# Kernel tuning notes

Measured on AMD Instinct MI355X. Metric: run time of the kernel, lower is better.

Reference implementation:

```python
import jax, jax.numpy as jnp
import numpy as np
from jax.scipy.special import ndtr, logsumexp

K = 2  # top-k experts (init kwarg k=2)


def setup_inputs() -> dict:
    key = jax.random.key(0)
    k1, k2, k3, k4 = jax.random.split(key, 4)
    B, D, E = 131072, 1024, 64
    x_flat = jax.random.normal(k1, (B, D), jnp.float32)
    # Original inits w_gate/w_noise to zeros; use small random weights so
    # top-k routing is non-degenerate for correctness testing.
    w_gate = jax.random.normal(k2, (D, E), jnp.float32) * 0.02
    w_noise = jax.random.normal(k3, (D, E), jnp.float32) * 0.02
    eps = jax.random.normal(k4, (B, E), jnp.float32)  # reified torch.randn_like
    return {"x_flat": x_flat, "w_gate": w_gate, "w_noise": w_noise, "eps": eps}


def _cv_squared(v):
    # torch .var() is unbiased (ddof=1)
    return jnp.var(v, ddof=1) / (jnp.mean(v) ** 2 + 1e-10)


def reference(x_flat, w_gate, w_noise, eps):
    B = x_flat.shape[0]
    clean_logits = x_flat @ w_gate                                  # [B, E]
    noise_stddev = jax.nn.softplus(x_flat @ w_noise) + 0.01         # [B, E]
    logits = clean_logits + eps * noise_stddev                      # noisy logits (training)

    top_vals, top_idx = jax.lax.top_k(logits, K + 1)                # [B, K+1], sorted desc
    top_k_gates = jax.nn.softmax(top_vals[:, :K], axis=-1)          # [B, K]
    gates = jnp.zeros_like(logits).at[jnp.arange(B)[:, None], top_idx[:, :K]].set(top_k_gates)

    # _prob_in_top_k load estimate (noisy gating, k < num_experts, training)
    thr_if_in = top_vals[:, K:K + 1]                                # (k+1)-th largest
    thr_if_out = top_vals[:, K - 1:K]                               # k-th largest
    is_in = logits > thr_if_in
    prob_if_in = ndtr((clean_logits - thr_if_in) / noise_stddev)
    prob_if_out = ndtr((clean_logits - thr_if_out) / noise_stddev)
    load = jnp.where(is_in, prob_if_in, prob_if_out).sum(0)         # [E]

    importance = gates.sum(0)                                       # [E]
    z_loss = logsumexp(logits, axis=-1).mean()                      # log(sum(exp)).mean()
    load_balancing = _cv_squared(importance) + _cv_squared(load) + z_loss
    return gates, load, logits, load_balancing, importance
```

## Files before the change

kernel.cpp:

```cpp
#include <hip/hip_runtime.h>
#include <math.h>

#define B_ROWS 131072
#define D_DIM  1024
#define E_EXP  64
#define MARGIN 4e-3f

typedef _Float16 f16;
typedef _Float16 f16x8 __attribute__((ext_vector_type(8)));
typedef float    f32x4 __attribute__((ext_vector_type(4)));

#define AS1C(p) ((const __attribute__((address_space(1))) void*)(p))
#define AS3(p)  ((__attribute__((address_space(3))) void*)(p))


__device__ __forceinline__ float softplus_f(float t) {
  return (t > 20.0f) ? t : log1pf(expf(t));
}
__device__ __forceinline__ float ndtr_f(float z) {
  return 0.5f * erfcf(-z * 0.70710678118654752f);
}
__device__ __forceinline__ void argmax64(float& v, int& vi) {
  #pragma unroll
  for (int off = 32; off > 0; off >>= 1) {
    float ov = __shfl_xor(v, off, 64);
    int   oi = __shfl_xor(vi, off, 64);
    if (ov > v || (ov == v && oi < vi)) { v = ov; vi = oi; }
  }
}
__device__ __forceinline__ float sum64(float v) {
  #pragma unroll
  for (int off = 32; off > 0; off >>= 1) v += __shfl_xor(v, off, 64);
  return v;
}

__device__ __forceinline__ void row_epilogue_exact(
    int row, int lane, float clean, float sd, float l,
    float* __restrict__ gates_buf, float* __restrict__ logits_buf,
    float& load_acc, float& imp_acc, float& z_acc)
{
  float v1 = l; int i1 = lane; argmax64(v1, i1);
  float v2 = (lane == i1) ? -INFINITY : l; int i2 = lane; argmax64(v2, i2);
  float v3 = (lane == i1 || lane == i2) ? -INFINITY : l; int i3 = lane; argmax64(v3, i3);
  (void)i3;
  const float e21 = expf(v2 - v1);
  const float g1  = 1.0f / (1.0f + e21);
  const float g2  = e21 * g1;
  const float gv  = (lane == i1) ? g1 : ((lane == i2) ? g2 : 0.0f);
  gates_buf [(size_t)row * E_EXP + lane] = gv;
  logits_buf[(size_t)row * E_EXP + lane] = l;
  const float ssum = sum64(expf(l - v1));
  z_acc += v1 + logf(ssum);
  const float thr = (l > v3) ? v3 : v2;
  load_acc += ndtr_f((clean - thr) / sd);
  imp_acc  += gv;
}


__global__ void init_acc(float* load_o, float* imp_o, float* zsum, int* flagcnt) {
  int t = threadIdx.x;
  if (t < 64) { load_o[t] = 0.0f; imp_o[t] = 0.0f; }
  if (t == 64) zsum[0] = 0.0f;
  if (t == 65) flagcnt[0] = 0;
}

__global__ __launch_bounds__(256) void prep_wt(
    const float* __restrict__ wg, const float* __restrict__ wn, f16* __restrict__ wt) {
  __shared__ float tile[64][65];
  const int m  = blockIdx.x >> 4;
  const int kt = blockIdx.x & 15;
  const int k0 = kt * 64;
  const float* src = m ? wn : wg;
  const int c = threadIdx.x & 63;
  const int r0 = threadIdx.x >> 6;
  #pragma unroll
  for (int r = r0; r < 64; r += 4)
    tile[r][c] = src[(size_t)(k0 + r) * 64 + c];
  __syncthreads();
  const int j = threadIdx.x & 63;
  #pragma unroll
  for (int col = r0; col < 64; col += 4)
    wt[(size_t)(m * 64 + col) * 1024 + k0 + j] = (f16)tile[j][col];
}

__global__ __launch_bounds__(256, 3) void gemm_fused(
    const float* __restrict__ x, const f16* __restrict__ wt,
    const float* __restrict__ eps,
    float* __restrict__ gates_buf, float* __restrict__ logits_buf,
    float* __restrict__ load_o, float* __restrict__ imp_o, float* __restrict__ zsum,
    int* __restrict__ flagcnt, int* __restrict__ flaglist)
{
  __shared__ __align__(16) char wlds[2][16384];

  const int tid  = threadIdx.x;
  const int lane = tid & 63;
  const int wid  = tid >> 6;
  const int l15  = lane & 15;
  const int l4   = lane >> 4;
  const size_t rowbase = (size_t)blockIdx.x * 128 + wid * 32;

  const int scol0 = wid * 8 + (lane >> 3);
  const int skel  = ((lane & 7) * 8) ^ ((lane >> 3) << 3);
  const f16* wsrc0 = wt + (size_t)(scol0 +  0) * 1024 + skel;
  const f16* wsrc1 = wt + (size_t)(scol0 + 32) * 1024 + skel;
  const f16* wsrc2 = wt + (size_t)(scol0 + 64) * 1024 + skel;
  const f16* wsrc3 = wt + (size_t)(scol0 + 96) * 1024 + skel;

#define ISSUE_B(buf, kc) do {                                                                      \
    __builtin_amdgcn_global_load_lds(AS1C(wsrc0 + (kc) * 64), AS3(&wlds[buf][0*4096 + wid*1024]), 16, 0, 0); \
    __builtin_amdgcn_global_load_lds(AS1C(wsrc1 + (kc) * 64), AS3(&wlds[buf][1*4096 + wid*1024]), 16, 0, 0); \
    __builtin_amdgcn_global_load_lds(AS1C(wsrc2 + (kc) * 64), AS3(&wlds[buf][2*4096 + wid*1024]), 16, 0, 0); \
    __builtin_amdgcn_global_load_lds(AS1C(wsrc3 + (kc) * 64), AS3(&wlds[buf][3*4096 + wid*1024]), 16, 0, 0); \
  } while (0)

  const float* xp0 = x + (rowbase +  0 + l15) * D_DIM + l4 * 8;
  const float* xp1 = x + (rowbase + 16 + l15) * D_DIM + l4 * 8;

  f32x4 acc[2][8];
  #pragma unroll
  for (int rt = 0; rt < 2; ++rt)
    #pragma unroll
    for (int et = 0; et < 8; ++et) acc[rt][et] = (f32x4)0.0f;

  float4 xa[8];
#define LOAD_A(kc) do {                                                  \
    _Pragma("unroll")                                                    \
    for (int kl = 0; kl < 2; ++kl) {                                     \
      xa[kl*4 + 0] = *(const float4*)(xp0 + (kc)*64 + kl*32 + 0);        \
      xa[kl*4 + 1] = *(const float4*)(xp0 + (kc)*64 + kl*32 + 4);        \
      xa[kl*4 + 2] = *(const float4*)(xp1 + (kc)*64 + kl*32 + 0);        \
      xa[kl*4 + 3] = *(const float4*)(xp1 + (kc)*64 + kl*32 + 4);        \
    }                                                                    \
  } while (0)

  ISSUE_B(0, 0);
  LOAD_A(0);
  __syncthreads();

  #pragma unroll 1
  for (int kc = 0; kc < 16; ++kc) {
    const int buf = kc & 1;

    f16x8 af[2][2];
    #pragma unroll
    for (int kl = 0; kl < 2; ++kl)
      #pragma unroll
      for (int rt = 0; rt < 2; ++rt) {
        #pragma unroll
        for (int h = 0; h < 2; ++h) {
          const float4 v = xa[kl*4 + rt*2 + h];
          af[kl][rt][h*4 + 0] = (f16)v.x;
          af[kl][rt][h*4 + 1] = (f16)v.y;
          af[kl][rt][h*4 + 2] = (f16)v.z;
          af[kl][rt][h*4 + 3] = (f16)v.w;
        }
      }

    if (kc < 15) {
      ISSUE_B(buf ^ 1, kc + 1);
      LOAD_A(kc + 1);
    }

    #pragma unroll
    for (int kl = 0; kl < 2; ++kl) {
      #pragma unroll
      for (int et = 0; et < 8; ++et) {
        const int bcol = et * 16 + l15;
        const int boff = (bcol * 128 + kl * 64 + l4 * 16) ^ ((l15 & 7) << 4);
        const f16x8 b = *(const f16x8*)(&wlds[buf][boff]);
        acc[0][et] = __builtin_amdgcn_mfma_f32_16x16x32_f16(af[kl][0], b, acc[0][et], 0, 0, 0);
        acc[1][et] = __builtin_amdgcn_mfma_f32_16x16x32_f16(af[kl][1], b, acc[1][et], 0, 0, 0);
      }
    }

    __syncthreads();
  }
#undef ISSUE_B
#undef LOAD_A

  float load_acc[4] = {0.f, 0.f, 0.f, 0.f};
  float imp_acc[4]  = {0.f, 0.f, 0.f, 0.f};
  float z_acc = 0.f;

  #pragma unroll
  for (int rt = 0; rt < 2; ++rt) {
    #pragma unroll
    for (int rg = 0; rg < 4; ++rg) {
      const size_t row = rowbase + rt * 16 + l4 * 4 + rg;
      float cl[4], sd[4], lg[4];
      #pragma unroll
      for (int j = 0; j < 4; ++j) {
        cl[j] = acc[rt][j][rg];
        sd[j] = softplus_f(acc[rt][4 + j][rg]) + 0.01f;
        const float ev = eps[row * E_EXP + j * 16 + l15];
        lg[j] = fmaf(ev, sd[j], cl[j]);
      }
      float v = lg[0]; int c = l15;
      #pragma unroll
      for (int j = 1; j < 4; ++j) {
        const int cj = j * 16 + l15;
        if (lg[j] > v || (lg[j] == v && cj < c)) { v = lg[j]; c = cj; }
      }
      #pragma unroll
      for (int off = 1; off < 16; off <<= 1) {
        const float ov = __shfl_xor(v, off, 64);
        const int   oc = __shfl_xor(c, off, 64);
        if (ov > v || (ov == v && oc < c)) { v = ov; c = oc; }
      }
      const float v1 = v; const int i1 = c;
      v = -INFINITY; c = 1 << 30;
      #pragma unroll
      for (int j = 0; j < 4; ++j) {
        const int cj = j * 16 + l15;
        if (cj != i1 && (lg[j] > v || (lg[j] == v && cj < c))) { v = lg[j]; c = cj; }
      }
      #pragma unroll
      for (int off = 1; off < 16; off <<= 1) {
        const float ov = __shfl_xor(v, off, 64);
        const int   oc = __shfl_xor(c, off, 64);
        if (ov > v || (ov == v && oc < c)) { v = ov; c = oc; }
      }
      const float v2 = v; const int i2 = c;
      float v3 = -INFINITY;
      #pragma unroll
      for (int j = 0; j < 4; ++j) {
        const int cj = j * 16 + l15;
        if (cj != i1 && cj != i2) v3 = fmaxf(v3, lg[j]);
      }
      #pragma unroll
      for (int off = 1; off < 16; off <<= 1) v3 = fmaxf(v3, __shfl_xor(v3, off, 64));

      if (v2 - v3 >= MARGIN) {
        const float e21 = expf(v2 - v1);
        const float g1  = 1.0f / (1.0f + e21);
        const float g2  = e21 * g1;
        float s = 0.f;
        #pragma unroll
        for (int j = 0; j < 4; ++j) s += expf(lg[j] - v1);
        #pragma unroll
        for (int off = 1; off < 16; off <<= 1) s += __shfl_xor(s, off, 64);
        if (l15 == 0) z_acc += v1 + logf(s);
        #pragma unroll
        for (int j = 0; j < 4; ++j) {
          const int cj = j * 16 + l15;
          const float gv = (cj == i1) ? g1 : ((cj == i2) ? g2 : 0.0f);
          gates_buf [row * E_EXP + cj] = gv;
          logits_buf[row * E_EXP + cj] = lg[j];
          imp_acc[j] += gv;
          const float thr = (lg[j] > v3) ? v3 : v2;
          load_acc[j] += ndtr_f((cl[j] - thr) / sd[j]);
        }
      } else {
        if (l15 == 0) { const int idx = atomicAdd(flagcnt, 1); flaglist[idx] = (int)row; }
      }
    }
  }

  float* red = (float*)&wlds[0][0];
  #pragma unroll
  for (int j = 0; j < 4; ++j) {
    float L = load_acc[j]; L += __shfl_xor(L, 16, 64); L += __shfl_xor(L, 32, 64);
    float I = imp_acc[j];  I += __shfl_xor(I, 16, 64); I += __shfl_xor(I, 32, 64);
    if (l4 == 0) {
      red[wid * 64 + j * 16 + l15]       = L;
      red[256 + wid * 64 + j * 16 + l15] = I;
    }
  }
  {
    const float zw = sum64(z_acc);
    if (lane == 0) red[512 + wid] = zw;
  }
  __syncthreads();
  if (wid == 0) {
    const float L = red[lane] + red[64 + lane] + red[128 + lane] + red[192 + lane];
    const float I = red[256 + lane] + red[320 + lane] + red[384 + lane] + red[448 + lane];
    atomicAdd(&load_o[lane], L);
    atomicAdd(&imp_o[lane],  I);
    if (lane == 0) atomicAdd(zsum, red[512] + red[513] + red[514] + red[515]);
  }
}

__global__ __launch_bounds__(256) void fixup_k(
    const float* __restrict__ x, const float* __restrict__ wg, const float* __restrict__ wn,
    const float* __restrict__ eps,
    float* __restrict__ gates_buf, float* __restrict__ logits_buf,
    float* __restrict__ load_o, float* __restrict__ imp_o, float* __restrict__ zsum,
    const int* __restrict__ flagcnt, const int* __restrict__ flaglist)
{
  const int lane = threadIdx.x & 63;
  const int wid  = threadIdx.x >> 6;
  __shared__ float redg[4][4][64], redn[4][4][64];

  const int nf = *flagcnt;

  for (int it = blockIdx.x * 4; it < nf; it += gridDim.x * 4) {
    const int nr = (nf - it < 4) ? (nf - it) : 4;
    int rows[4];
    #pragma unroll
    for (int rr = 0; rr < 4; ++rr) rows[rr] = flaglist[it + ((rr < nr) ? rr : 0)];

    float dg[4] = {0.f,0.f,0.f,0.f}, dn[4] = {0.f,0.f,0.f,0.f};
    const int dbase = wid * 256;
    for (int d = 0; d < 256; d += 4) {
      const int db = (dbase + d) * E_EXP + lane;
      const float wgv0 = wg[db], wgv1 = wg[db + 64], wgv2 = wg[db + 128], wgv3 = wg[db + 192];
      const float wnv0 = wn[db], wnv1 = wn[db + 64], wnv2 = wn[db + 128], wnv3 = wn[db + 192];
      #pragma unroll
      for (int rr = 0; rr < 4; ++rr) {
        const float4 xv = *(const float4*)(x + (size_t)rows[rr] * D_DIM + dbase + d);
        dg[rr] = fmaf(xv.x, wgv0, dg[rr]);  dn[rr] = fmaf(xv.x, wnv0, dn[rr]);
        dg[rr] = fmaf(xv.y, wgv1, dg[rr]);  dn[rr] = fmaf(xv.y, wnv1, dn[rr]);
        dg[rr] = fmaf(xv.z, wgv2, dg[rr]);  dn[rr] = fmaf(xv.z, wnv2, dn[rr]);
        dg[rr] = fmaf(xv.w, wgv3, dg[rr]);  dn[rr] = fmaf(xv.w, wnv3, dn[rr]);
      }
    }
    #pragma unroll
    for (int rr = 0; rr < 4; ++rr) { redg[wid][rr][lane] = dg[rr]; redn[wid][rr][lane] = dn[rr]; }
    __syncthreads();
    if (wid < nr) {
      const int row = rows[wid];
      const float clean = redg[0][wid][lane] + redg[1][wid][lane] + redg[2][wid][lane] + redg[3][wid][lane];
      const float sdraw = redn[0][wid][lane] + redn[1][wid][lane] + redn[2][wid][lane] + redn[3][wid][lane];
      const float sd = softplus_f(sdraw) + 0.01f;
      const float ev = eps[(size_t)row * E_EXP + lane];
      const float l  = fmaf(ev, sd, clean);
      float la = 0.f, ia = 0.f, za = 0.f;
      row_epilogue_exact(row, lane, clean, sd, l, gates_buf, logits_buf, la, ia, za);
      atomicAdd(&load_o[lane], la);
      atomicAdd(&imp_o[lane],  ia);
      if (lane == 0) atomicAdd(zsum, za);
    }
    __syncthreads();
  }
}

__global__ void finalize_k(const float* __restrict__ load_o,
                           const float* __restrict__ imp_o,
                           const float* __restrict__ zsum,
                           float* __restrict__ out_lb) {
  if (threadIdx.x == 0 && blockIdx.x == 0) {
    double sl = 0.0, sl2 = 0.0, si = 0.0, si2 = 0.0;
    for (int e = 0; e < E_EXP; ++e) {
      double a = (double)load_o[e]; sl += a; sl2 += a * a;
      double b = (double)imp_o[e];  si += b; si2 += b * b;
    }
    const double n  = (double)E_EXP;
    const double ml = sl / n, mi = si / n;
    const double varl = (sl2 - n * ml * ml) / (n - 1.0);
    const double vari = (si2 - n * mi * mi) / (n - 1.0);
    const double cvl = varl / (ml * ml + 1e-10);
    const double cvi = vari / (mi * mi + 1e-10);
    const double z  = (double)zsum[0] / (double)B_ROWS;
    out_lb[0] = (float)(cvi + cvl + z);
  }
}


extern "C" void kernel_launch(void* const* d_in, const int* in_sizes, int n_in,
                              void* d_out, int out_size, void* d_ws, size_t ws_size,
                              hipStream_t stream) {
  const float* x   = (const float*)d_in[0];
  const float* wg  = (const float*)d_in[1];
  const float* wn  = (const float*)d_in[2];
  const float* eps = (const float*)d_in[3];

  float* out    = (float*)d_out;
  float* gates  = out;
  float* load_o = out + (size_t)B_ROWS * E_EXP;
  float* logits = load_o + E_EXP;
  float* lb     = logits + (size_t)B_ROWS * E_EXP;
  float* imp    = lb + 1;

  float* zsum     = (float*)d_ws;
  int*   flagcnt  = (int*)d_ws + 2;
  int*   flaglist = (int*)((char*)d_ws + 256);
  f16*   wt       = (f16*)((char*)d_ws + 256 + 4 * (size_t)B_ROWS);

  init_acc<<<1, 128, 0, stream>>>(load_o, imp, zsum, flagcnt);
  prep_wt<<<32, 256, 0, stream>>>(wg, wn, wt);
  gemm_fused<<<B_ROWS / 128, 256, 0, stream>>>(
      x, wt, eps, gates, logits, load_o, imp, zsum, flagcnt, flaglist);
  fixup_k<<<512, 256, 0, stream>>>(x, wg, wn, eps, gates, logits, load_o, imp, zsum, flagcnt, flaglist);
  finalize_k<<<1, 64, 0, stream>>>(load_o, imp, zsum, lb);
}
```

Measured before the change: 271.3 us.

## Load GEMM weight fragments directly from global memory instead of LDS staging

Result: slower. 311.0 us (+14.6%).

```diff
diff --git a/kernel.cpp b/kernel.cpp
--- a/kernel.cpp
+++ b/kernel.cpp
@@ -9,9 +9,6 @@
 typedef _Float16 f16;
 typedef _Float16 f16x8 __attribute__((ext_vector_type(8)));
 typedef float    f32x4 __attribute__((ext_vector_type(4)));
-
-#define AS1C(p) ((const __attribute__((address_space(1))) void*)(p))
-#define AS3(p)  ((__attribute__((address_space(3))) void*)(p))
 
 
 __device__ __forceinline__ float softplus_f(float t) {
@@ -57,15 +54,15 @@
 }
 
 
-__global__ void init_acc(float* load_o, float* imp_o, float* zsum, int* flagcnt) {
-  int t = threadIdx.x;
-  if (t < 64) { load_o[t] = 0.0f; imp_o[t] = 0.0f; }
-  if (t == 64) zsum[0] = 0.0f;
-  if (t == 65) flagcnt[0] = 0;
-}
-
 __global__ __launch_bounds__(256) void prep_wt(
-    const float* __restrict__ wg, const float* __restrict__ wn, f16* __restrict__ wt) {
+    const float* __restrict__ wg, const float* __restrict__ wn, f16* __restrict__ wt,
+    float* load_o, float* imp_o, float* zsum, int* flagcnt) {
+  if (blockIdx.x == 0) {
+    const int t = threadIdx.x;
+    if (t < 64) { load_o[t] = 0.0f; imp_o[t] = 0.0f; }
+    if (t == 64) zsum[0] = 0.0f;
+    if (t == 65) flagcnt[0] = 0;
+  }
   __shared__ float tile[64][65];
   const int m  = blockIdx.x >> 4;
   const int kt = blockIdx.x & 15;
@@ -83,14 +80,14 @@
     wt[(size_t)(m * 64 + col) * 1024 + k0 + j] = (f16)tile[j][col];
 }
 
-__global__ __launch_bounds__(256, 3) void gemm_fused(
+__global__ __launch_bounds__(256, 2) void gemm_fused(
     const float* __restrict__ x, const f16* __restrict__ wt,
     const float* __restrict__ eps,
     float* __restrict__ gates_buf, float* __restrict__ logits_buf,
     float* __restrict__ load_o, float* __restrict__ imp_o, float* __restrict__ zsum,
     int* __restrict__ flagcnt, int* __restrict__ flaglist)
 {
-  __shared__ __align__(16) char wlds[2][16384];
+  __shared__ float red[520];
 
   const int tid  = threadIdx.x;
   const int lane = tid & 63;
@@ -99,19 +96,7 @@
   const int l4   = lane >> 4;
   const size_t rowbase = (size_t)blockIdx.x * 128 + wid * 32;
 
-  const int scol0 = wid * 8 + (lane >> 3);
-  const int skel  = ((lane & 7) * 8) ^ ((lane >> 3) << 3);
-  const f16* wsrc0 = wt + (size_t)(scol0 +  0) * 1024 + skel;
-  const f16* wsrc1 = wt + (size_t)(scol0 + 32) * 1024 + skel;
-  const f16* wsrc2 = wt + (size_t)(scol0 + 64) * 1024 + skel;
-  const f16* wsrc3 = wt + (size_t)(scol0 + 96) * 1024 + skel;
-
-#define ISSUE_B(buf, kc) do {                                                                      \
-    __builtin_amdgcn_global_load_lds(AS1C(wsrc0 + (kc) * 64), AS3(&wlds[buf][0*4096 + wid*1024]), 16, 0, 0); \
-    __builtin_amdgcn_global_load_lds(AS1C(wsrc1 + (kc) * 64), AS3(&wlds[buf][1*4096 + wid*1024]), 16, 0, 0); \
-    __builtin_amdgcn_global_load_lds(AS1C(wsrc2 + (kc) * 64), AS3(&wlds[buf][2*4096 + wid*1024]), 16, 0, 0); \
-    __builtin_amdgcn_global_load_lds(AS1C(wsrc3 + (kc) * 64), AS3(&wlds[buf][3*4096 + wid*1024]), 16, 0, 0); \
-  } while (0)
+  const f16* wb = wt + (size_t)l15 * 1024 + l4 * 8;
 
   const float* xp0 = x + (rowbase +  0 + l15) * D_DIM + l4 * 8;
   const float* xp1 = x + (rowbase + 16 + l15) * D_DIM + l4 * 8;
@@ -133,13 +118,17 @@
     }                                                                    \
   } while (0)
 
-  ISSUE_B(0, 0);
   LOAD_A(0);
-  __syncthreads();
 
   #pragma unroll 1
   for (int kc = 0; kc < 16; ++kc) {
-    const int buf = kc & 1;
+    f16x8 b[8][2];
+    #pragma unroll
+    for (int et = 0; et < 8; ++et) {
+      #pragma unroll
+      for (int kl = 0; kl < 2; ++kl)
+        b[et][kl] = *(const f16x8*)(wb + (size_t)et * 16384 + kc * 64 + kl * 32);
+    }
 
     f16x8 af[2][2];
     #pragma unroll
@@ -156,26 +145,17 @@
         }
       }
 
-    if (kc < 15) {
-      ISSUE_B(buf ^ 1, kc + 1);
-      LOAD_A(kc + 1);
-    }
+    if (kc < 15) LOAD_A(kc + 1);
 
     #pragma unroll
     for (int kl = 0; kl < 2; ++kl) {
       #pragma unroll
       for (int et = 0; et < 8; ++et) {
-        const int bcol = et * 16 + l15;
-        const int boff = (bcol * 128 + kl * 64 + l4 * 16) ^ ((l15 & 7) << 4);
-        const f16x8 b = *(const f16x8*)(&wlds[buf][boff]);
-        acc[0][et] = __builtin_amdgcn_mfma_f32_16x16x32_f16(af[kl][0], b, acc[0][et], 0, 0, 0);
-        acc[1][et] = __builtin_amdgcn_mfma_f32_16x16x32_f16(af[kl][1], b, acc[1][et], 0, 0, 0);
-      }
-    }
-
-    __syncthreads();
-  }
-#undef ISSUE_B
+        acc[0][et] = __builtin_amdgcn_mfma_f32_16x16x32_f16(af[kl][0], b[et][kl], acc[0][et], 0, 0, 0);
+        acc[1][et] = __builtin_amdgcn_mfma_f32_16x16x32_f16(af[kl][1], b[et][kl], acc[1][et], 0, 0, 0);
+      }
+    }
+  }
 #undef LOAD_A
 
   float load_acc[4] = {0.f, 0.f, 0.f, 0.f};
@@ -256,7 +236,6 @@
     }
   }
 
-  float* red = (float*)&wlds[0][0];
   #pragma unroll
   for (int j = 0; j < 4; ++j) {
     float L = load_acc[j]; L += __shfl_xor(L, 16, 64); L += __shfl_xor(L, 32, 64);
@@ -338,12 +317,18 @@
                            const float* __restrict__ imp_o,
                            const float* __restrict__ zsum,
                            float* __restrict__ out_lb) {
-  if (threadIdx.x == 0 && blockIdx.x == 0) {
-    double sl = 0.0, sl2 = 0.0, si = 0.0, si2 = 0.0;
-    for (int e = 0; e < E_EXP; ++e) {
-      double a = (double)load_o[e]; sl += a; sl2 += a * a;
-      double b = (double)imp_o[e];  si += b; si2 += b * b;
-    }
+  const int e = threadIdx.x & 63;
+  const double a = (double)load_o[e];
+  const double b = (double)imp_o[e];
+  double sl = a, sl2 = a * a, si = b, si2 = b * b;
+  #pragma unroll
+  for (int off = 32; off > 0; off >>= 1) {
+    sl  += __shfl_xor(sl,  off, 64);
+    sl2 += __shfl_xor(sl2, off, 64);
+    si  += __shfl_xor(si,  off, 64);
+    si2 += __shfl_xor(si2, off, 64);
+  }
+  if (e == 0) {
     const double n  = (double)E_EXP;
     const double ml = sl / n, mi = si / n;
     const double varl = (sl2 - n * ml * ml) / (n - 1.0);
@@ -376,8 +361,7 @@
   int*   flaglist = (int*)((char*)d_ws + 256);
   f16*   wt       = (f16*)((char*)d_ws + 256 + 4 * (size_t)B_ROWS);
 
-  init_acc<<<1, 128, 0, stream>>>(load_o, imp, zsum, flagcnt);
-  prep_wt<<<32, 256, 0, stream>>>(wg, wn, wt);
+  prep_wt<<<32, 256, 0, stream>>>(wg, wn, wt, load_o, imp, zsum, flagcnt);
   gemm_fused<<<B_ROWS / 128, 256, 0, stream>>>(
       x, wt, eps, gates, logits, load_o, imp, zsum, flagcnt, flaglist);
   fixup_k<<<512, 256, 0, stream>>>(x, wg, wn, eps, gates, logits, load_o, imp, zsum, flagcnt, flaglist);
```

## Issue weight prefetch earlier and wait only on LDS loads at barriers

Applied to the files above, without the earlier changes.

Result: no change. 274.0 us (+1.0%).

```diff
diff --git a/kernel.cpp b/kernel.cpp
--- a/kernel.cpp
+++ b/kernel.cpp
@@ -57,15 +57,15 @@
 }
 
 
-__global__ void init_acc(float* load_o, float* imp_o, float* zsum, int* flagcnt) {
-  int t = threadIdx.x;
-  if (t < 64) { load_o[t] = 0.0f; imp_o[t] = 0.0f; }
-  if (t == 64) zsum[0] = 0.0f;
-  if (t == 65) flagcnt[0] = 0;
-}
-
 __global__ __launch_bounds__(256) void prep_wt(
-    const float* __restrict__ wg, const float* __restrict__ wn, f16* __restrict__ wt) {
+    const float* __restrict__ wg, const float* __restrict__ wn, f16* __restrict__ wt,
+    float* load_o, float* imp_o, float* zsum, int* flagcnt) {
+  if (blockIdx.x == 0) {
+    const int t = threadIdx.x;
+    if (t < 64) { load_o[t] = 0.0f; imp_o[t] = 0.0f; }
+    if (t == 64) zsum[0] = 0.0f;
+    if (t == 65) flagcnt[0] = 0;
+  }
   __shared__ float tile[64][65];
   const int m  = blockIdx.x >> 4;
   const int kt = blockIdx.x & 15;
@@ -111,6 +111,12 @@
     __builtin_amdgcn_global_load_lds(AS1C(wsrc1 + (kc) * 64), AS3(&wlds[buf][1*4096 + wid*1024]), 16, 0, 0); \
     __builtin_amdgcn_global_load_lds(AS1C(wsrc2 + (kc) * 64), AS3(&wlds[buf][2*4096 + wid*1024]), 16, 0, 0); \
     __builtin_amdgcn_global_load_lds(AS1C(wsrc3 + (kc) * 64), AS3(&wlds[buf][3*4096 + wid*1024]), 16, 0, 0); \
+  } while (0)
+
+#define PIPE_BARRIER() do {                                  \
+    asm volatile("s_waitcnt vmcnt(8)" ::: "memory");         \
+    __builtin_amdgcn_s_barrier();                            \
+    __builtin_amdgcn_sched_barrier(0);                       \
   } while (0)
 
   const float* xp0 = x + (rowbase +  0 + l15) * D_DIM + l4 * 8;
@@ -135,11 +141,13 @@
 
   ISSUE_B(0, 0);
   LOAD_A(0);
-  __syncthreads();
+  PIPE_BARRIER();
 
   #pragma unroll 1
   for (int kc = 0; kc < 16; ++kc) {
     const int buf = kc & 1;
+
+    if (kc < 15) ISSUE_B(buf ^ 1, kc + 1);
 
     f16x8 af[2][2];
     #pragma unroll
@@ -156,10 +164,7 @@
         }
       }
 
-    if (kc < 15) {
-      ISSUE_B(buf ^ 1, kc + 1);
-      LOAD_A(kc + 1);
-    }
+    if (kc < 15) LOAD_A(kc + 1);
 
     #pragma unroll
     for (int kl = 0; kl < 2; ++kl) {
@@ -173,10 +178,11 @@
       }
     }
 
-    __syncthreads();
+    if (kc < 15) PIPE_BARRIER();
   }
 #undef ISSUE_B
 #undef LOAD_A
+#undef PIPE_BARRIER
 
   float load_acc[4] = {0.f, 0.f, 0.f, 0.f};
   float imp_acc[4]  = {0.f, 0.f, 0.f, 0.f};
@@ -338,12 +344,18 @@
                            const float* __restrict__ imp_o,
                            const float* __restrict__ zsum,
                            float* __restrict__ out_lb) {
-  if (threadIdx.x == 0 && blockIdx.x == 0) {
-    double sl = 0.0, sl2 = 0.0, si = 0.0, si2 = 0.0;
-    for (int e = 0; e < E_EXP; ++e) {
-      double a = (double)load_o[e]; sl += a; sl2 += a * a;
-      double b = (double)imp_o[e];  si += b; si2 += b * b;
-    }
+  const int e = threadIdx.x & 63;
+  const double a = (double)load_o[e];
+  const double b = (double)imp_o[e];
+  double sl = a, sl2 = a * a, si = b, si2 = b * b;
+  #pragma unroll
+  for (int off = 32; off > 0; off >>= 1) {
+    sl  += __shfl_xor(sl,  off, 64);
+    sl2 += __shfl_xor(sl2, off, 64);
+    si  += __shfl_xor(si,  off, 64);
+    si2 += __shfl_xor(si2, off, 64);
+  }
+  if (e == 0) {
     const double n  = (double)E_EXP;
     const double ml = sl / n, mi = si / n;
     const double varl = (sl2 - n * ml * ml) / (n - 1.0);
@@ -376,8 +388,7 @@
   int*   flaglist = (int*)((char*)d_ws + 256);
   f16*   wt       = (f16*)((char*)d_ws + 256 + 4 * (size_t)B_ROWS);
 
-  init_acc<<<1, 128, 0, stream>>>(load_o, imp, zsum, flagcnt);
-  prep_wt<<<32, 256, 0, stream>>>(wg, wn, wt);
+  prep_wt<<<32, 256, 0, stream>>>(wg, wn, wt, load_o, imp, zsum, flagcnt);
   gemm_fused<<<B_ROWS / 128, 256, 0, stream>>>(
       x, wt, eps, gates, logits, load_o, imp, zsum, flagcnt, flaglist);
   fixup_k<<<512, 256, 0, stream>>>(x, wg, wn, eps, gates, logits, load_o, imp, zsum, flagcnt, flaglist);
```
